# Kernel tuning notes

Hardware: AMD Instinct MI355X
Metric: run time of the kernel (lower is better)

## Reference

```python
import jax, jax.numpy as jnp
import numpy as np

DIMS = 2048
HEAD_DIM = 64
NUM_HEADS = DIMS // HEAD_DIM   # 32
GQA_HEADS = 2                  # KV heads
EPS = 1e-8


def setup_inputs() -> dict:
    key = jax.random.key(0)
    ks = jax.random.split(key, 6)
    b, s = 2, 2048
    kv_dims = HEAD_DIM * GQA_HEADS  # 128
    x = jax.random.normal(ks[0], (b, s, DIMS), dtype=jnp.float32)
    Wq = jax.random.normal(ks[1], (DIMS, DIMS), dtype=jnp.float32) * 0.02
    Wk = jax.random.normal(ks[2], (kv_dims, DIMS), dtype=jnp.float32) * 0.02
    Wv = jax.random.normal(ks[3], (kv_dims, DIMS), dtype=jnp.float32) * 0.02
    Wo = jax.random.normal(ks[4], (DIMS, DIMS), dtype=jnp.float32) * 0.02
    norm_scale = jnp.ones((DIMS,), dtype=jnp.float32)           # RMSNorm.scale
    split_scale = jnp.full((DIMS,), 0.1, dtype=jnp.float32)     # RMS_split.scale
    return {"x": x, "norm_scale": norm_scale, "split_scale": split_scale,
            "Wq": Wq, "Wk": Wk, "Wv": Wv, "Wo": Wo}


def reference(x, norm_scale, split_scale, Wq, Wk, Wv, Wo):
    b, s, d = x.shape
    H, G, dh = NUM_HEADS, GQA_HEADS, HEAD_DIM
    hpg = H // G  # query heads per KV group

    # RMS_split pre-norm: RMSNorm (l2-norm based) then elementwise scale
    nrm = jnp.linalg.norm(x, axis=-1, keepdims=True) * (d ** -0.5)
    h = (norm_scale * x / (nrm + EPS)) * split_scale

    # projections (nn.Linear with weight [out, in], no bias)
    q = (h @ Wq.T).reshape(b, s, H, dh)          # b s H dh
    k = (h @ Wk.T).reshape(b, s, G, dh)          # b s G dh
    v = (h @ Wv.T).reshape(b, s, G, dh)

    # group query heads: b G hpg s dh
    q = q.transpose(0, 2, 1, 3).reshape(b, G, hpg, s, dh)
    k = k.transpose(0, 2, 1, 3)                  # b G s dh
    v = v.transpose(0, 2, 1, 3)                  # b G s dh

    scores = jnp.einsum('bghsd,bgtd->bghst', q, k) / np.float32(np.sqrt(dh))
    attn = jax.nn.softmax(scores, axis=-1)
    out = jnp.einsum('bghst,bgtd->bghsd', attn, v)   # b G hpg s dh

    out = out.reshape(b, H, s, dh).transpose(0, 2, 1, 3).reshape(b, s, H * dh)
    return x + out @ Wo.T
```

## Files before the change

kernel.cpp:

```cpp
#include <hip/hip_runtime.h>

typedef unsigned short u16;
typedef unsigned int u32;
typedef __bf16 bf16x8 __attribute__((ext_vector_type(8)));
typedef float f32x4 __attribute__((ext_vector_type(4)));

#define DIMS 2048
#define SEQ 2048
#define BATCH 2
#define NH 32
#define NG 2
#define DH 64
#define MROWS (BATCH * SEQ)
#define KVD (NG * DH)

#define SCL2 (0.125f * 1.44269504088896f)

__device__ __forceinline__ u16 f2bf(float f) {
  u32 u = __float_as_uint(f);
  u32 r = u + 0x7fffu + ((u >> 16) & 1u);
  return (u16)(r >> 16);
}
__device__ __forceinline__ u32 pack2(float a, float b) {
  return (u32)f2bf(a) | ((u32)f2bf(b) << 16);
}
__device__ __forceinline__ u32 cvtpk(float a, float b) {
#if __has_builtin(__builtin_amdgcn_cvt_pk_bf16_f32)
  typedef __bf16 bf16x2 __attribute__((ext_vector_type(2)));
  union {
    bf16x2 v;
    u32 u;
  } r;
  r.v = __builtin_amdgcn_cvt_pk_bf16_f32(a, b);
  return r.u;
#else
  return pack2(a, b);
#endif
}
__device__ __forceinline__ void glds16(const u16* g, u16* l) {
  __builtin_amdgcn_global_load_lds(
      (const __attribute__((address_space(1))) void*)g,
      (__attribute__((address_space(3))) void*)l, 16, 0, 0);
}

__global__ __launch_bounds__(256) void rms_split_kernel(
    const float* __restrict__ x, const float* __restrict__ ns,
    const float* __restrict__ ss, u16* __restrict__ h) {
  const int row = blockIdx.x;
  const int tid = threadIdx.x;
  const float* xr = x + (size_t)row * DIMS;
  float4 v0 = ((const float4*)xr)[tid];
  float4 v1 = ((const float4*)xr)[tid + 256];
  float s = v0.x * v0.x + v0.y * v0.y + v0.z * v0.z + v0.w * v0.w +
            v1.x * v1.x + v1.y * v1.y + v1.z * v1.z + v1.w * v1.w;
#pragma unroll
  for (int d = 1; d < 64; d <<= 1) s += __shfl_xor(s, d, 64);
  __shared__ float red[4];
  if ((tid & 63) == 0) red[tid >> 6] = s;
  __syncthreads();
  float tot = red[0] + red[1] + red[2] + red[3];
  float inv = 1.0f / (sqrtf(tot * (1.0f / DIMS)) + 1e-8f);
  float4 a0 = ((const float4*)ns)[tid];
  float4 a1 = ((const float4*)ns)[tid + 256];
  float4 b0 = ((const float4*)ss)[tid];
  float4 b1 = ((const float4*)ss)[tid + 256];
  uint2 o0, o1;
  o0.x = pack2(v0.x * a0.x * b0.x * inv, v0.y * a0.y * b0.y * inv);
  o0.y = pack2(v0.z * a0.z * b0.z * inv, v0.w * a0.w * b0.w * inv);
  o1.x = pack2(v1.x * a1.x * b1.x * inv, v1.y * a1.y * b1.y * inv);
  o1.y = pack2(v1.z * a1.z * b1.z * inv, v1.w * a1.w * b1.w * inv);
  uint2* hr = (uint2*)(h + (size_t)row * DIMS);
  hr[tid] = o0;
  hr[tid + 256] = o1;
}

__global__ __launch_bounds__(256) void cvt2_kernel(const float* __restrict__ a,
                                                   u16* __restrict__ oa,
                                                   const float* __restrict__ b,
                                                   u16* __restrict__ ob,
                                                   int half) {
  const int bx = blockIdx.x;
  const float* src = bx < half ? a : b;
  u16* dst = bx < half ? oa : ob;
  const int i = (bx < half ? bx : bx - half) * 256 + threadIdx.x;
  float4 v = ((const float4*)src)[i];
  uint2 r;
  r.x = pack2(v.x, v.y);
  r.y = pack2(v.z, v.w);
  ((uint2*)dst)[i] = r;
}

template <int MODE>
__global__ __launch_bounds__(256) void gemm_bt(
    const u16* __restrict__ A, const u16* __restrict__ B, void* __restrict__ Cv,
    const float* __restrict__ R, u16* __restrict__ kb, u16* __restrict__ vtb,
    int M, int N, int K) {
  __shared__ u16 As[128 * 32];
  __shared__ u16 Bs[128 * 32];
  const int tid = threadIdx.x;
  const int lane = tid & 63;
  const int wv = tid >> 6;
  const int fr = lane & 15;
  const int fq = lane >> 4;
  const int m0 = blockIdx.y * 128;
  const int n0 = blockIdx.x * 128;
  const int wm = wv & 1;
  const int wn = wv >> 1;

  const int srow = tid >> 2;
  const int scol = (tid & 3) * 8;
  const u16* Ag0 = A + (size_t)(m0 + srow) * K + scol;
  const u16* Ag1 = A + (size_t)(m0 + srow + 64) * K + scol;
  const u16* Bg0 = B + (size_t)(n0 + srow) * K + scol;
  const u16* Bg1 = B + (size_t)(n0 + srow + 64) * K + scol;
  u16* Al0 = As + wv * 512;
  u16* Al1 = As + 2048 + wv * 512;
  u16* Bl0 = Bs + wv * 512;
  u16* Bl1 = Bs + 2048 + wv * 512;

  f32x4 acc[4][4];
#pragma unroll
  for (int i = 0; i < 4; ++i)
#pragma unroll
    for (int j = 0; j < 4; ++j)
#pragma unroll
      for (int e = 0; e < 4; ++e) acc[i][j][e] = 0.0f;

  const u16* ap[4];
  const u16* bp[4];
#pragma unroll
  for (int i = 0; i < 4; ++i) {
    ap[i] = As + (wm * 64 + i * 16 + fr) * 32 + fq * 8;
    bp[i] = Bs + (wn * 64 + i * 16 + fr) * 32 + fq * 8;
  }

  for (int k0 = 0; k0 < K; k0 += 32) {
    glds16(Ag0 + k0, Al0);
    glds16(Ag1 + k0, Al1);
    glds16(Bg0 + k0, Bl0);
    glds16(Bg1 + k0, Bl1);
    __syncthreads();
    bf16x8 af[4], bf[4];
#pragma unroll
    for (int i = 0; i < 4; ++i) {
      af[i] = *(const bf16x8*)ap[i];
      bf[i] = *(const bf16x8*)bp[i];
    }
#pragma unroll
    for (int i = 0; i < 4; ++i)
#pragma unroll
      for (int j = 0; j < 4; ++j)
        acc[i][j] = __builtin_amdgcn_mfma_f32_16x16x32_bf16(af[i], bf[j],
                                                            acc[i][j], 0, 0, 0);
    __syncthreads();
  }

#pragma unroll
  for (int i = 0; i < 4; ++i) {
    const int m = m0 + wm * 64 + i * 16 + fq * 4;
#pragma unroll
    for (int j = 0; j < 4; ++j) {
      const int n = n0 + wn * 64 + j * 16 + fr;
#pragma unroll
      for (int r = 0; r < 4; ++r) {
        if (MODE == 1) {
          const size_t idx = (size_t)(m + r) * N + n;
          ((float*)Cv)[idx] = R[idx] + acc[i][j][r];
        } else {
          if (n0 < 2048)
            ((u16*)Cv)[(size_t)(m + r) * DIMS + n] = f2bf(acc[i][j][r]);
          else if (n0 < 2176)
            kb[(size_t)(m + r) * KVD + (n - 2048)] = f2bf(acc[i][j][r] * SCL2);
          else
            vtb[(size_t)(n - 2176) * MROWS + (m + r)] = f2bf(acc[i][j][r]);
        }
      }
    }
  }
}

__global__ __launch_bounds__(256, 4) void attn_kernel(
    const u16* __restrict__ q, const u16* __restrict__ kbuf,
    const u16* __restrict__ vT, u16* __restrict__ out) {
  __shared__ u16 Ks[2][8 * 512];
  __shared__ u16 Vs[2][8 * 512];
  const int tid = threadIdx.x;
  const int lane = tid & 63;
  const int wv = tid >> 6;
  const int fr = lane & 15;
  const int fq = lane >> 4;
  const int b = blockIdx.x >> 5;
  const int hq = blockIdx.x & 31;
  const int g = hq >> 4;
  const int q0 = blockIdx.y * 128 + wv * 32;

  bf16x8 af[2][2];
#pragma unroll
  for (int mt = 0; mt < 2; ++mt)
#pragma unroll
    for (int kx = 0; kx < 2; ++kx)
      af[mt][kx] =
          *(const bf16x8*)(q + (size_t)(b * SEQ + q0 + mt * 16 + fr) * DIMS +
                           hq * DH + kx * 32 + fq * 8);

  f32x4 Oa[2][4];
  f32x4 On[2];
#pragma unroll
  for (int mt = 0; mt < 2; ++mt) {
#pragma unroll
    for (int e = 0; e < 4; ++e) On[mt][e] = 0.0f;
#pragma unroll
    for (int j = 0; j < 4; ++j)
#pragma unroll
      for (int e = 0; e < 4; ++e) Oa[mt][j][e] = 0.0f;
  }

  bf16x8 onev;
#pragma unroll
  for (int e = 0; e < 8; ++e) onev[e] = (__bf16)1.0f;

  const int kk =
      (lane & 32) | ((lane & 16) >> 2) | ((lane & 12) << 1) | (lane & 3);
  const u16* ksrc = kbuf + (size_t)(b * SEQ + kk) * KVD + g * DH;
  const u16* vsrc = vT + (size_t)(g * DH + lane) * MROWS + b * SEQ;

  const int c0 = wv * 2;
#define STAGE(buf, tile)                                                     \
  {                                                                          \
    const int t0_ = (tile)*64;                                               \
    _Pragma("unroll") for (int s = 0; s < 2; ++s) {                          \
      const int c = c0 + s;                                                  \
      glds16(ksrc + (size_t)t0_ * KVD + (c >> 2) * 32 + (c & 3) * 8,         \
             &Ks[buf][c * 512]);                                             \
      glds16(vsrc + t0_ + c * 8, &Vs[buf][c * 512]);                         \
    }                                                                        \
  }

#define COMPUTE(buf)                                                          \
  {                                                                           \
    _Pragma("unroll") for (int kg = 0; kg < 2; ++kg) {                        \
      bf16x8 kf00 = *(const bf16x8*)(&Ks[buf][fq * 512 + (kg * 32 + fr) * 8]); \
      bf16x8 kf01 =                                                           \
          *(const bf16x8*)(&Ks[buf][(4 + fq) * 512 + (kg * 32 + fr) * 8]);    \
      bf16x8 kf10 =                                                           \
          *(const bf16x8*)(&Ks[buf][fq * 512 + (kg * 32 + 16 + fr) * 8]);     \
      bf16x8 kf11 = *(const bf16x8*)(&Ks[buf][(4 + fq) * 512 +                \
                                              (kg * 32 + 16 + fr) * 8]);      \
      bf16x8 vf[4];                                                           \
      _Pragma("unroll") for (int jt = 0; jt < 4; ++jt) vf[jt] =               \
          *(const bf16x8*)(&Vs[buf][(kg * 4 + fq) * 512 + (jt * 16 + fr) * 8]); \
      _Pragma("unroll") for (int mt = 0; mt < 2; ++mt) {                      \
        f32x4 s0 = {0.0f, 0.0f, 0.0f, 0.0f};                                  \
        f32x4 s1 = {0.0f, 0.0f, 0.0f, 0.0f};                                  \
        s0 = __builtin_amdgcn_mfma_f32_16x16x32_bf16(kf00, af[mt][0], s0, 0,  \
                                                     0, 0);                   \
        s0 = __builtin_amdgcn_mfma_f32_16x16x32_bf16(kf01, af[mt][1], s0, 0,  \
                                                     0, 0);                   \
        s1 = __builtin_amdgcn_mfma_f32_16x16x32_bf16(kf10, af[mt][0], s1, 0,  \
                                                     0, 0);                   \
        s1 = __builtin_amdgcn_mfma_f32_16x16x32_bf16(kf11, af[mt][1], s1, 0,  \
                                                     0, 0);                   \
        const float p0 = __builtin_amdgcn_exp2f(s0[0]);                       \
        const float p1 = __builtin_amdgcn_exp2f(s0[1]);                       \
        const float p2 = __builtin_amdgcn_exp2f(s0[2]);                       \
        const float p3 = __builtin_amdgcn_exp2f(s0[3]);                       \
        const float p4 = __builtin_amdgcn_exp2f(s1[0]);                       \
        const float p5 = __builtin_amdgcn_exp2f(s1[1]);                       \
        const float p6 = __builtin_amdgcn_exp2f(s1[2]);                       \
        const float p7 = __builtin_amdgcn_exp2f(s1[3]);                       \
        union {                                                               \
          bf16x8 v;                                                           \
          u32 u[4];                                                           \
        } pu;                                                                 \
        pu.u[0] = cvtpk(p0, p1);                                              \
        pu.u[1] = cvtpk(p2, p3);                                              \
        pu.u[2] = cvtpk(p4, p5);                                              \
        pu.u[3] = cvtpk(p6, p7);                                              \
        _Pragma("unroll") for (int jt = 0; jt < 4; ++jt) Oa[mt][jt] =         \
            __builtin_amdgcn_mfma_f32_16x16x32_bf16(pu.v, vf[jt], Oa[mt][jt], \
                                                    0, 0, 0);                 \
        On[mt] = __builtin_amdgcn_mfma_f32_16x16x32_bf16(pu.v, onev, On[mt],  \
                                                         0, 0, 0);            \
      }                                                                       \
    }                                                                         \
  }

  STAGE(0, 0);
  for (int it = 0; it < 32; it += 2) {
    STAGE(1, (it + 1) & 31);
    asm volatile("s_waitcnt vmcnt(4)\ns_barrier" ::: "memory");
    COMPUTE(0);
    asm volatile("s_barrier" ::: "memory");
    STAGE(0, (it + 2) & 31);
    asm volatile("s_waitcnt vmcnt(4)\ns_barrier" ::: "memory");
    COMPUTE(1);
    asm volatile("s_barrier" ::: "memory");
  }
#undef STAGE
#undef COMPUTE

#pragma unroll
  for (int mt = 0; mt < 2; ++mt)
#pragma unroll
    for (int r = 0; r < 4; ++r) {
      const float invl = 1.0f / On[mt][r];
      const int row = q0 + mt * 16 + fq * 4 + r;
#pragma unroll
      for (int jt = 0; jt < 4; ++jt)
        out[(size_t)(b * SEQ + row) * DIMS + hq * DH + jt * 16 + fr] =
            f2bf(Oa[mt][jt][r] * invl);
    }
}

extern "C" void kernel_launch(void* const* d_in, const int* in_sizes, int n_in,
                              void* d_out, int out_size, void* d_ws,
                              size_t ws_size, hipStream_t stream) {
  const float* x = (const float*)d_in[0];
  const float* ns = (const float*)d_in[1];
  const float* ssc = (const float*)d_in[2];
  const float* Wq = (const float*)d_in[3];
  const float* Wk = (const float*)d_in[4];
  const float* Wv = (const float*)d_in[5];
  const float* Wo = (const float*)d_in[6];

  char* ws = (char*)d_ws;
  u16* hbuf = (u16*)(ws);
  u16* bqkv = (u16*)(ws + 16777216);
  u16* bWo = (u16*)(ws + 26214400);
  u16* qb = (u16*)(ws + 34603008);
  u16* kb = (u16*)(ws + 51380224);
  u16* vtb = (u16*)(ws + 52428800);
  u16* ab = (u16*)(ws + 53477376);

  rms_split_kernel<<<dim3(4096), dim3(256), 0, stream>>>(x, ns, ssc, hbuf);
  cvt2_kernel<<<dim3(8192), dim3(256), 0, stream>>>(Wq, bqkv, Wo, bWo, 4096);
  cvt2_kernel<<<dim3(512), dim3(256), 0, stream>>>(
      Wk, bqkv + (size_t)2048 * 2048, Wv, bqkv + (size_t)2176 * 2048, 256);

  gemm_bt<2><<<dim3(18, 32), dim3(256), 0, stream>>>(
      hbuf, bqkv, qb, nullptr, kb, vtb, 4096, 2048, 2048);
  attn_kernel<<<dim3(64, 16), dim3(256), 0, stream>>>(qb, kb, vtb, ab);
  gemm_bt<1><<<dim3(16, 32), dim3(256), 0, stream>>>(
      ab, bWo, d_out, x, nullptr, nullptr, 4096, 2048, 2048);
}
```

Baseline: 337.8 us.

## Store K and V in pre-tiled LDS-image layout for contiguous attention staging

The projection GEMM epilogue now writes K and V directly into a per-(batch,group,tile,chunk) layout that matches the LDS image the attention kernel expects, with the lane permutation baked in. Attention staging then becomes fully contiguous 16-byte-per-lane loads instead of strided gathers from row-major K and the transposed V. This replaces scattered global loads in the attention loop with scattered stores in the GEMM epilogue, which may hurt that epilogue's coalescing.

```diff
diff --git a/kernel.cpp b/kernel.cpp
--- a/kernel.cpp
+++ b/kernel.cpp
@@ -167,12 +167,34 @@
           const size_t idx = (size_t)(m + r) * N + n;
           ((float*)Cv)[idx] = R[idx] + acc[i][j][r];
         } else {
-          if (n0 < 2048)
+          if (n0 < 2048) {
             ((u16*)Cv)[(size_t)(m + r) * DIMS + n] = f2bf(acc[i][j][r]);
-          else if (n0 < 2176)
-            kb[(size_t)(m + r) * KVD + (n - 2048)] = f2bf(acc[i][j][r] * SCL2);
-          else
-            vtb[(size_t)(n - 2176) * MROWS + (m + r)] = f2bf(acc[i][j][r]);
+          } else {
+            const int token = m + r;
+            const int bb = token >> 11;
+            const int srw = token & 2047;
+            const int t = srw >> 6;
+            const int rowin = srw & 63;
+            if (n0 < 2176) {
+              const int d = n - 2048;
+              const int gg = d >> 6;
+              const int dd = d & 63;
+              const int c = ((dd >> 5) << 2) | ((dd >> 3) & 3);
+              const int jj = dd & 7;
+              const int pos = (rowin & 32) | ((rowin & 4) << 2) |
+                              ((rowin & 0x18) >> 1) | (rowin & 3);
+              kb[(((size_t)(bb * NG + gg) * 32 + t) * 8 + c) * 512 + pos * 8 +
+                 jj] = f2bf(acc[i][j][r] * SCL2);
+            } else {
+              const int d = n - 2176;
+              const int gg = d >> 6;
+              const int dv = d & 63;
+              const int c = rowin >> 3;
+              const int jj = rowin & 7;
+              vtb[(((size_t)(bb * NG + gg) * 32 + t) * 8 + c) * 512 + dv * 8 +
+                  jj] = f2bf(acc[i][j][r]);
+            }
+          }
         }
       }
     }
@@ -219,21 +241,18 @@
 #pragma unroll
   for (int e = 0; e < 8; ++e) onev[e] = (__bf16)1.0f;
 
-  const int kk =
-      (lane & 32) | ((lane & 16) >> 2) | ((lane & 12) << 1) | (lane & 3);
-  const u16* ksrc = kbuf + (size_t)(b * SEQ + kk) * KVD + g * DH;
-  const u16* vsrc = vT + (size_t)(g * DH + lane) * MROWS + b * SEQ;
+  const u16* ksrc = kbuf + (size_t)(b * NG + g) * 32 * 4096;
+  const u16* vsrc = vT + (size_t)(b * NG + g) * 32 * 4096;
 
   const int c0 = wv * 2;
-#define STAGE(buf, tile)                                                     \
-  {                                                                          \
-    const int t0_ = (tile)*64;                                               \
-    _Pragma("unroll") for (int s = 0; s < 2; ++s) {                          \
-      const int c = c0 + s;                                                  \
-      glds16(ksrc + (size_t)t0_ * KVD + (c >> 2) * 32 + (c & 3) * 8,         \
-             &Ks[buf][c * 512]);                                             \
-      glds16(vsrc + t0_ + c * 8, &Vs[buf][c * 512]);                         \
-    }                                                                        \
+#define STAGE(buf, tile)                                     \
+  {                                                          \
+    const size_t tb_ = (size_t)(tile)*4096;                  \
+    _Pragma("unroll") for (int s = 0; s < 2; ++s) {          \
+      const int c = c0 + s;                                  \
+      glds16(ksrc + tb_ + c * 512 + lane * 8, &Ks[buf][c * 512]); \
+      glds16(vsrc + tb_ + c * 512 + lane * 8, &Vs[buf][c * 512]); \
+    }                                                        \
   }
 
 #define COMPUTE(buf)                                                          \
```

After: 331.0 us. 1.02x faster.
